# Performance work log

Measured on AMD Instinct MI355X. Metric: run time of the kernel, lower is better.

Reference implementation:

```python
import jax, jax.numpy as jnp
import numpy as np

B, T = 256, 800
D_IN, H, L, V = 128, 512, 2, 128


def setup_inputs() -> dict:
    key = jax.random.key(0)
    ks = jax.random.split(key, 12)
    s = 0.1  # init scale for stability
    return {
        "W_ih0": jax.random.normal(ks[0], (4 * H, D_IN), jnp.float32) * s,
        "W_hh0": jax.random.normal(ks[1], (4 * H, H), jnp.float32) * s,
        "b_ih0": jax.random.normal(ks[2], (4 * H,), jnp.float32) * s,
        "b_hh0": jax.random.normal(ks[3], (4 * H,), jnp.float32) * s,
        "W_ih1": jax.random.normal(ks[4], (4 * H, H), jnp.float32) * s,
        "W_hh1": jax.random.normal(ks[5], (4 * H, H), jnp.float32) * s,
        "b_ih1": jax.random.normal(ks[6], (4 * H,), jnp.float32) * s,
        "b_hh1": jax.random.normal(ks[7], (4 * H,), jnp.float32) * s,
        "W_lin": jax.random.normal(ks[8], (V, H), jnp.float32) * s,
        "b_lin": jax.random.normal(ks[9], (V,), jnp.float32) * s,
        "z": jax.random.randint(ks[10], (B, T), 0, V, jnp.int32),
        "num_frames": jax.random.randint(ks[11], (B,), 100, 800, jnp.int32),
    }


def _lstm_log_prob(layers, W_lin, b_lin, z, num_frames):
    # teacher-forced inputs: step i sees one_hot(z[:, i-1]), zeros at i=0
    oh = jax.nn.one_hot(z[:, :-1], D_IN, dtype=jnp.float32)          # [B, T-1, D]
    inputs = jnp.concatenate([jnp.zeros((B, 1, D_IN), jnp.float32), oh], axis=1)
    inputs = jnp.transpose(inputs, (1, 0, 2))                         # [T, B, D]

    def step(carry, x_t):
        h, c = carry  # each [L, B, H]
        inp = x_t
        hs, cs = [], []
        for l, (Wih, Whh, bih, bhh) in enumerate(layers):
            gates = inp @ Wih.T + h[l] @ Whh.T + bih + bhh            # [B, 4H]
            i, f, g, o = jnp.split(gates, 4, axis=-1)                 # torch gate order i,f,g,o
            c_new = jax.nn.sigmoid(f) * c[l] + jax.nn.sigmoid(i) * jnp.tanh(g)
            h_new = jax.nn.sigmoid(o) * jnp.tanh(c_new)
            hs.append(h_new)
            cs.append(c_new)
            inp = h_new
        logits_t = inp @ W_lin.T + b_lin                              # [B, V]
        return (jnp.stack(hs), jnp.stack(cs)), logits_t

    h0 = jnp.zeros((L, B, H), jnp.float32)
    c0 = jnp.zeros((L, B, H), jnp.float32)
    _, logits = jax.lax.scan(step, (h0, c0), inputs)                  # [T, B, V]
    logits = jnp.transpose(logits, (1, 0, 2))                         # [B, T, V]

    logp = jax.nn.log_softmax(logits, axis=-1)
    nll = -jnp.take_along_axis(logp, z[..., None].astype(jnp.int32), axis=-1)[..., 0]  # [B, T]
    mask = (jnp.arange(T)[None, :] < num_frames[:, None]).astype(nll.dtype)
    return (nll * mask).mean(axis=-1)                                 # [B] (mean over full T, as in torch)


def reference(W_ih0, W_hh0, b_ih0, b_hh0, W_ih1, W_hh1, b_ih1, b_hh1, W_lin, b_lin, z, num_frames):
    layers = [(W_ih0, W_hh0, b_ih0, b_hh0), (W_ih1, W_hh1, b_ih1, b_hh1)]
    return _lstm_log_prob(layers, W_lin, b_lin, z, num_frames)
```

## Files before the change

kernel.cpp:

```cpp
#include <hip/hip_runtime.h>

#define TT 800

typedef __attribute__((ext_vector_type(8))) short bf16x8;
typedef __attribute__((ext_vector_type(4))) float f32x4;
typedef unsigned short u16;
typedef unsigned int u32;
typedef unsigned long long u64;

constexpr int NCW = 128, NWG = 136, RT = 32;
constexpr size_t WL0A_OFF = 0;
constexpr size_t WL0B_OFF = 2097152;
constexpr size_t WL1_OFF  = 2621440;
constexpr size_t WLIN_OFF = 6815744;
constexpr size_t H0_OFF   = 6946816;
constexpr size_t H1_OFF   = 7471104;
constexpr size_t BAR_OFF  = 7995392;
constexpr int HB = 256 * 512;
constexpr int A_ST = 520;
constexpr int G_OFF_B = 33280;
constexpr int P_OFF_B = 49792;
constexpr int LDS_BYTES = 53248;

__device__ __forceinline__ u16 f2b(float x) {
  u32 u = __float_as_uint(x);
  return (u16)((u + 0x7FFFu + ((u >> 16) & 1u)) >> 16);
}
__device__ __forceinline__ float b2f(u16 v) { return __uint_as_float(((u32)v) << 16); }
__device__ __forceinline__ float sigf(float x) { return 1.f / (1.f + __expf(-x)); }
__device__ __forceinline__ float tanh_f(float x) { float e = __expf(2.f * x); return 1.f - 2.f / (e + 1.f); }

__device__ __forceinline__ u64 ld_coh8(const u64* p) {
  return __hip_atomic_load(p, __ATOMIC_RELAXED, __HIP_MEMORY_SCOPE_AGENT);
}
__device__ __forceinline__ void st_coh8(u64* p, u64 v) {
  __hip_atomic_store(p, v, __ATOMIC_RELAXED, __HIP_MEMORY_SCOPE_AGENT);
}
__device__ __forceinline__ void fadd(u32* f) {
  __hip_atomic_fetch_add(f, 1u, __ATOMIC_RELAXED, __HIP_MEMORY_SCOPE_AGENT);
}
__device__ __forceinline__ void fpoll(u32* f, u32 thr) {
  while (__hip_atomic_load(f, __ATOMIC_RELAXED, __HIP_MEMORY_SCOPE_AGENT) < thr)
    __builtin_amdgcn_s_sleep(1);
}

__global__ void prep_kernel(const float* __restrict__ wih0, const float* __restrict__ whh0,
                            const float* __restrict__ wih1, const float* __restrict__ whh1,
                            const float* __restrict__ wlinf,
                            u16* __restrict__ wl0a, u16* __restrict__ wl0b,
                            u16* __restrict__ wl1, u16* __restrict__ wlin) {
  int i = blockIdx.x * 256 + threadIdx.x;
  const int NA = 2048 * 512, NB = 128 * 2048, N1 = 2048 * 1024, N2 = 128 * 512;
  if (i < NA) {
    int col = i >> 9, k = i & 511;
    wl0a[i] = f2b(whh0[col * 512 + k]);
  } else if (i < NA + NB) {
    int j = i - NA, k = j >> 11, col = j & 2047;
    wl0b[j] = f2b(wih0[col * 128 + k]);
  } else if (i < NA + NB + N1) {
    int j = i - NA - NB, col = j >> 10, k = j & 1023;
    float v = (k < 512) ? wih1[col * 512 + k] : whh1[col * 512 + (k - 512)];
    wl1[j] = f2b(v);
  } else if (i < NA + NB + N1 + N2) {
    int j = i - NA - NB - N1, col = j >> 9, k = j & 511;
    wlin[j] = f2b(wlinf[col * 512 + k]);
  }
}

__global__ __launch_bounds__(256, 1) void lstm_kernel(
    const float* __restrict__ bih0, const float* __restrict__ bhh0,
    const float* __restrict__ bih1, const float* __restrict__ bhh1,
    const float* __restrict__ blin,
    const int* __restrict__ z, const int* __restrict__ nfr,
    const u16* __restrict__ wl0a, const u16* __restrict__ wl0b,
    const u16* __restrict__ wl1, const u16* __restrict__ wlin,
    u16* __restrict__ h0buf, u16* __restrict__ h1buf,
    u32* __restrict__ bars, float* __restrict__ out) {
  extern __shared__ char smem[];
  u16* A = (u16*)smem;
  float* Gf = (float*)(smem + G_OFF_B);
  float* Pm = (float*)(smem + P_OFF_B);
  float* Ps = Pm + 256;
  float* Pt = Ps + 256;
  const int wg = blockIdx.x;
  const int w_all = wg >> 3;
  const bool isC = (w_all < 16);
  const int tile = wg & 7;
  const int w = isC ? w_all : 16;
  const int tid = threadIdx.x, lane = tid & 63, wv = tid >> 6;
  const int l15 = lane & 15, l4 = lane >> 4;
  const int row0 = tile * RT;
  u32* F = bars + tile * 32;
  const f32x4 VZ = {0.f, 0.f, 0.f, 0.f};
  const int rC = tid >> 3, u0C = (tid & 7) * 4;
  const int cuL = tid & 31, rgL = tid >> 5;

  float c0s[4] = {0, 0, 0, 0}, c1s[4] = {0, 0, 0, 0};
  float accN = 0.f, nflv = 0.f;
  float bias0c[2], bias1c[2], biasLc[2];
  bf16x8 bq0R[32];
  bf16x8 bq1R[64];
  bf16x8 wlR[32];

  if (isC) {
#pragma unroll
    for (int cb = 0; cb < 2; ++cb) {
      int col = wv * 512 + w * 32 + cb * 16 + l15;
      bias0c[cb] = bih0[col] + bhh0[col];
      bias1c[cb] = bih1[col] + bhh1[col];
      const u16* b0 = wl0a + (size_t)col * 512 + l4 * 8;
#pragma unroll
      for (int kb = 0; kb < 16; ++kb) bq0R[cb * 16 + kb] = *(const bf16x8*)(b0 + kb * 32);
      const u16* b1 = wl1 + (size_t)col * 1024 + l4 * 8;
#pragma unroll
      for (int kb = 0; kb < 32; ++kb) bq1R[cb * 32 + kb] = *(const bf16x8*)(b1 + kb * 32);
    }
  } else {
#pragma unroll
    for (int cb = 0; cb < 2; ++cb) {
      int colV = wv * 32 + cb * 16 + l15;
      biasLc[cb] = blin[colV];
      const u16* bL = wlin + (size_t)colV * 512 + l4 * 8;
#pragma unroll
      for (int kb = 0; kb < 16; ++kb) wlR[cb * 16 + kb] = *(const bf16x8*)(bL + kb * 32);
    }
    if (rgL == 0) nflv = (float)nfr[row0 + cuL];
  }

  if (isC && w == 0) {
    u64* z0 = (u64*)(h0buf + HB + row0 * 512);
    u64* z1 = (u64*)(h1buf + row0 * 512);
    u64* z2 = (u64*)(h1buf + HB + row0 * 512);
    for (int k = tid; k < 2048; k += 256) { st_coh8(z0 + k, 0); st_coh8(z1 + k, 0); st_coh8(z2 + k, 0); }
  }
  __syncthreads();
  if (tid == 0) fadd(F);

  auto ldA = [&](int rb, int kb) {
    return *(const bf16x8*)(A + (rb * 16 + l15) * A_ST + kb * 32 + l4 * 8);
  };

#pragma unroll 1
  for (int tau = 0; tau <= TT + 1; ++tau) {
    if (tid == 0) fpoll(F, 17u * (u32)(tau + 1));
    __syncthreads();
    const u16* h0src = h0buf + ((tau + 1) & 1) * HB + row0 * 512;
    const u64* h1s64 = (const u64*)(h1buf + (tau & 1) * HB + row0 * 512);
    const bool l0act = isC && (tau < TT);
    const bool l1act = isC && (tau >= 1 && tau <= TT);

    if (isC) {
      if (tau <= TT) {
        u64 ta[8], tb[8];
        const u64* s64 = (const u64*)h0src;
#pragma unroll
        for (int c = 0; c < 8; ++c) {
          int li = c * 256 + tid;
          ta[c] = ld_coh8(s64 + li * 2); tb[c] = ld_coh8(s64 + li * 2 + 1);
        }
#pragma unroll
        for (int c = 0; c < 8; ++c) {
          int li = c * 256 + tid, row = li >> 6, cc = li & 63;
          u64* d = (u64*)(A + row * A_ST + cc * 8);
          d[0] = ta[c]; d[1] = tb[c];
        }
      }
      u64 ha[4], hb[4];
      if (l1act) {
#pragma unroll
        for (int c = 0; c < 4; ++c) {
          int li = c * 256 + tid;
          ha[c] = ld_coh8(h1s64 + li * 2); hb[c] = ld_coh8(h1s64 + li * 2 + 1);
        }
      }
      __syncthreads();

      f32x4 acc0[2][2] = {{VZ, VZ}, {VZ, VZ}};
      f32x4 acc1[2][2] = {{VZ, VZ}, {VZ, VZ}};
      if (l0act) {
#pragma unroll
        for (int kb = 0; kb < 16; ++kb) {
          bf16x8 a0 = ldA(0, kb), a1 = ldA(1, kb);
#pragma unroll
          for (int cb = 0; cb < 2; ++cb) {
            acc0[0][cb] = __builtin_amdgcn_mfma_f32_16x16x32_bf16(a0, bq0R[cb * 16 + kb], acc0[0][cb], 0, 0, 0);
            acc0[1][cb] = __builtin_amdgcn_mfma_f32_16x16x32_bf16(a1, bq0R[cb * 16 + kb], acc0[1][cb], 0, 0, 0);
          }
        }
      }
      if (l1act) {
#pragma unroll
        for (int kb = 0; kb < 16; ++kb) {
          bf16x8 a0 = ldA(0, kb), a1 = ldA(1, kb);
#pragma unroll
          for (int cb = 0; cb < 2; ++cb) {
            acc1[0][cb] = __builtin_amdgcn_mfma_f32_16x16x32_bf16(a0, bq1R[cb * 32 + kb], acc1[0][cb], 0, 0, 0);
            acc1[1][cb] = __builtin_amdgcn_mfma_f32_16x16x32_bf16(a1, bq1R[cb * 32 + kb], acc1[1][cb], 0, 0, 0);
          }
        }
      }
      if (l0act) {
#pragma unroll
        for (int rb = 0; rb < 2; ++rb)
#pragma unroll
          for (int cb = 0; cb < 2; ++cb)
#pragma unroll
            for (int q = 0; q < 4; ++q)
              Gf[(rb * 16 + l4 * 4 + q) * 129 + wv * 32 + cb * 16 + l15] = acc0[rb][cb][q] + bias0c[cb];
      }
      __syncthreads();

      u64 ha2[4], hb2[4];
      if (l1act) {
#pragma unroll
        for (int c = 0; c < 4; ++c) {
          int li = (c + 4) * 256 + tid;
          ha2[c] = ld_coh8(h1s64 + li * 2); hb2[c] = ld_coh8(h1s64 + li * 2 + 1);
        }
      }
      if (l0act) {
        float g4[4][4];
#pragma unroll
        for (int g = 0; g < 4; ++g)
#pragma unroll
          for (int j = 0; j < 4; ++j) g4[g][j] = Gf[rC * 129 + g * 32 + u0C + j];
        if (tau >= 1) {
          int zr = z[(row0 + rC) * TT + (tau - 1)];
          const u16* gb = wl0b + (size_t)zr * 2048 + w * 32 + u0C;
#pragma unroll
          for (int g = 0; g < 4; ++g) {
            u64 v = *(const u64*)(gb + g * 512);
#pragma unroll
            for (int j = 0; j < 4; ++j) g4[g][j] += b2f((u16)(v >> (16 * j)));
          }
        }
        u64 pk = 0;
#pragma unroll
        for (int j = 0; j < 4; ++j) {
          float cn = sigf(g4[1][j]) * c0s[j] + sigf(g4[0][j]) * tanh_f(g4[2][j]);
          float hn = sigf(g4[3][j]) * tanh_f(cn);
          c0s[j] = cn;
          pk |= ((u64)f2b(hn)) << (16 * j);
        }
        u16* h0w = h0buf + (tau & 1) * HB + row0 * 512;
        st_coh8((u64*)(h0w + rC * 512 + w * 32 + u0C), pk);
      }
      if (l1act) {
#pragma unroll
        for (int c = 0; c < 4; ++c) {
          int li = c * 256 + tid, row = li >> 6, cc = li & 63;
          u64* d = (u64*)(A + row * A_ST + cc * 8);
          d[0] = ha[c]; d[1] = hb[c];
        }
#pragma unroll
        for (int c = 0; c < 4; ++c) {
          int li = (c + 4) * 256 + tid, row = li >> 6, cc = li & 63;
          u64* d = (u64*)(A + row * A_ST + cc * 8);
          d[0] = ha2[c]; d[1] = hb2[c];
        }
      }
      __syncthreads();

      if (l1act) {
#pragma unroll
        for (int kb = 16; kb < 32; ++kb) {
          bf16x8 a0 = ldA(0, kb - 16), a1 = ldA(1, kb - 16);
#pragma unroll
          for (int cb = 0; cb < 2; ++cb) {
            acc1[0][cb] = __builtin_amdgcn_mfma_f32_16x16x32_bf16(a0, bq1R[cb * 32 + kb], acc1[0][cb], 0, 0, 0);
            acc1[1][cb] = __builtin_amdgcn_mfma_f32_16x16x32_bf16(a1, bq1R[cb * 32 + kb], acc1[1][cb], 0, 0, 0);
          }
        }
#pragma unroll
        for (int rb = 0; rb < 2; ++rb)
#pragma unroll
          for (int cb = 0; cb < 2; ++cb)
#pragma unroll
            for (int q = 0; q < 4; ++q)
              Gf[(rb * 16 + l4 * 4 + q) * 129 + wv * 32 + cb * 16 + l15] = acc1[rb][cb][q] + bias1c[cb];
      }
      __syncthreads();

      if (l1act) {
        float g4[4][4];
#pragma unroll
        for (int g = 0; g < 4; ++g)
#pragma unroll
          for (int j = 0; j < 4; ++j) g4[g][j] = Gf[rC * 129 + g * 32 + u0C + j];
        u64 pk = 0;
#pragma unroll
        for (int j = 0; j < 4; ++j) {
          float cn = sigf(g4[1][j]) * c1s[j] + sigf(g4[0][j]) * tanh_f(g4[2][j]);
          float hn = sigf(g4[3][j]) * tanh_f(cn);
          c1s[j] = cn;
          pk |= ((u64)f2b(hn)) << (16 * j);
        }
        u16* h1w = h1buf + ((tau + 1) & 1) * HB + row0 * 512;
        st_coh8((u64*)(h1w + rC * 512 + w * 32 + u0C), pk);
      }
      __syncthreads();
      if (tid == 0) fadd(F);
    } else {
      const bool lgact = (tau >= 2);
      if (lgact) {
        u64 ta[8], tb[8];
#pragma unroll
        for (int c = 0; c < 8; ++c) {
          int li = c * 256 + tid;
          ta[c] = ld_coh8(h1s64 + li * 2); tb[c] = ld_coh8(h1s64 + li * 2 + 1);
        }
#pragma unroll
        for (int c = 0; c < 8; ++c) {
          int li = c * 256 + tid, row = li >> 6, cc = li & 63;
          u64* d = (u64*)(A + row * A_ST + cc * 8);
          d[0] = ta[c]; d[1] = tb[c];
        }
      }
      __syncthreads();
      if (tid == 0) fadd(F);
      if (lgact) {
        f32x4 accL[2][2] = {{VZ, VZ}, {VZ, VZ}};
#pragma unroll
        for (int kb = 0; kb < 16; ++kb) {
          bf16x8 a0 = ldA(0, kb), a1 = ldA(1, kb);
#pragma unroll
          for (int cb = 0; cb < 2; ++cb) {
            accL[0][cb] = __builtin_amdgcn_mfma_f32_16x16x32_bf16(a0, wlR[cb * 16 + kb], accL[0][cb], 0, 0, 0);
            accL[1][cb] = __builtin_amdgcn_mfma_f32_16x16x32_bf16(a1, wlR[cb * 16 + kb], accL[1][cb], 0, 0, 0);
          }
        }
#pragma unroll
        for (int rb = 0; rb < 2; ++rb)
#pragma unroll
          for (int cb = 0; cb < 2; ++cb)
#pragma unroll
            for (int q = 0; q < 4; ++q)
              Gf[(rb * 16 + l4 * 4 + q) * 129 + wv * 32 + cb * 16 + l15] = accL[rb][cb][q] + biasLc[cb];
      }
      __syncthreads();
      if (lgact) {
        int t2 = tau - 2;
        int r = cuL, k = rgL;
        float vloc[16], mloc = -3.4e38f;
#pragma unroll
        for (int j = 0; j < 16; ++j) {
          vloc[j] = Gf[r * 129 + k * 16 + j];
          mloc = fmaxf(mloc, vloc[j]);
        }
        Pm[r * 8 + k] = mloc;
        __syncthreads();
        float mrow = Pm[r * 8];
#pragma unroll
        for (int j = 1; j < 8; ++j) mrow = fmaxf(mrow, Pm[r * 8 + j]);
        int zr = z[(row0 + r) * TT + t2];
        float sloc = 0.f, tloc = 0.f;
#pragma unroll
        for (int j = 0; j < 16; ++j) {
          sloc += __expf(vloc[j] - mrow);
          tloc += (k * 16 + j == zr) ? vloc[j] : 0.f;
        }
        Ps[r * 8 + k] = sloc; Pt[r * 8 + k] = tloc;
        __syncthreads();
        if (k == 0) {
          float s = 0.f, tv = 0.f;
#pragma unroll
          for (int j = 0; j < 8; ++j) { s += Ps[r * 8 + j]; tv += Pt[r * 8 + j]; }
          if ((float)t2 < nflv) accN += mrow + __logf(s) - tv;
        }
      } else {
        __syncthreads(); __syncthreads();
      }
    }
  }

  if (!isC && rgL == 0) out[row0 + cuL] = accN * (1.0f / TT);
}

extern "C" void kernel_launch(void* const* d_in, const int* in_sizes, int n_in,
                              void* d_out, int out_size, void* d_ws, size_t ws_size,
                              hipStream_t stream) {
  const float* wih0 = (const float*)d_in[0];
  const float* whh0 = (const float*)d_in[1];
  const float* bih0 = (const float*)d_in[2];
  const float* bhh0 = (const float*)d_in[3];
  const float* wih1 = (const float*)d_in[4];
  const float* whh1 = (const float*)d_in[5];
  const float* bih1 = (const float*)d_in[6];
  const float* bhh1 = (const float*)d_in[7];
  const float* wlinf = (const float*)d_in[8];
  const float* blin = (const float*)d_in[9];
  const int* z = (const int*)d_in[10];
  const int* nfr = (const int*)d_in[11];
  float* out = (float*)d_out;
  char* ws = (char*)d_ws;
  u16* wl0a = (u16*)(ws + WL0A_OFF);
  u16* wl0b = (u16*)(ws + WL0B_OFF);
  u16* wl1 = (u16*)(ws + WL1_OFF);
  u16* wlin = (u16*)(ws + WLIN_OFF);
  u16* h0buf = (u16*)(ws + H0_OFF);
  u16* h1buf = (u16*)(ws + H1_OFF);
  u32* bars = (u32*)(ws + BAR_OFF);

  hipMemsetAsync(ws + BAR_OFF, 0, 2048, stream);
  const int NTOT = 2048 * 512 + 128 * 2048 + 2048 * 1024 + 128 * 512;
  prep_kernel<<<dim3((NTOT + 255) / 256), dim3(256), 0, stream>>>(
      wih0, whh0, wih1, whh1, wlinf, wl0a, wl0b, wl1, wlin);
  lstm_kernel<<<dim3(NWG), dim3(256), LDS_BYTES, stream>>>(
      bih0, bhh0, bih1, bhh1, blin, z, nfr, wl0a, wl0b, wl1, wlin, h0buf, h1buf, bars, out);
}
```

Before: 8.631 ms.

## Use XCC-local coherence for per-tile flags and hidden-state exchange when co-located

```diff
diff --git a/kernel.cpp b/kernel.cpp
--- a/kernel.cpp
+++ b/kernel.cpp
@@ -43,6 +43,16 @@
   while (__hip_atomic_load(f, __ATOMIC_RELAXED, __HIP_MEMORY_SCOPE_AGENT) < thr)
     __builtin_amdgcn_s_sleep(1);
 }
+__device__ __forceinline__ void fadd_l(u32* f) {
+  __hip_atomic_fetch_add(f, 1u, __ATOMIC_RELAXED, __HIP_MEMORY_SCOPE_WORKGROUP);
+}
+__device__ __forceinline__ void fpoll_l(u32* f, u32 thr) {
+  while (*(volatile u32*)f < thr) {
+    __builtin_amdgcn_s_sleep(1);
+    asm volatile("buffer_inv" ::: "memory");
+  }
+}
+__device__ __forceinline__ void l1inv() { asm volatile("buffer_inv" ::: "memory"); }
 
 __global__ void prep_kernel(const float* __restrict__ wih0, const float* __restrict__ whh0,
                             const float* __restrict__ wih1, const float* __restrict__ whh1,
@@ -127,14 +137,37 @@
     if (rgL == 0) nflv = (float)nfr[row0 + cuL];
   }
 
+  u32 xcc;
+  asm volatile("s_getreg_b32 %0, hwreg(HW_REG_XCC_ID)" : "=s"(xcc));
+  {
+    int* hls = (int*)Pm;
+    if (tid == 0) {
+      u32 bit = 1u << (xcc & 31u);
+      __hip_atomic_fetch_or(bars + 256 + tile, bit, __ATOMIC_RELAXED, __HIP_MEMORY_SCOPE_AGENT);
+      __hip_atomic_fetch_add(bars + 272, 1u, __ATOMIC_RELAXED, __HIP_MEMORY_SCOPE_AGENT);
+      while (__hip_atomic_load(bars + 272, __ATOMIC_RELAXED, __HIP_MEMORY_SCOPE_AGENT) < (u32)NWG)
+        __builtin_amdgcn_s_sleep(1);
+      u32 m = __hip_atomic_load(bars + 256 + tile, __ATOMIC_RELAXED, __HIP_MEMORY_SCOPE_AGENT);
+      hls[0] = (m == bit) ? 1 : 0;
+    }
+    __syncthreads();
+    const_cast<volatile int&>(hls[0]);
+  }
+  const bool lok = (((volatile int*)Pm)[0] != 0);
+  __syncthreads();
+
   if (isC && w == 0) {
     u64* z0 = (u64*)(h0buf + HB + row0 * 512);
     u64* z1 = (u64*)(h1buf + row0 * 512);
     u64* z2 = (u64*)(h1buf + HB + row0 * 512);
-    for (int k = tid; k < 2048; k += 256) { st_coh8(z0 + k, 0); st_coh8(z1 + k, 0); st_coh8(z2 + k, 0); }
+    if (lok) {
+      for (int k = tid; k < 2048; k += 256) { z0[k] = 0; z1[k] = 0; z2[k] = 0; }
+    } else {
+      for (int k = tid; k < 2048; k += 256) { st_coh8(z0 + k, 0); st_coh8(z1 + k, 0); st_coh8(z2 + k, 0); }
+    }
   }
   __syncthreads();
-  if (tid == 0) fadd(F);
+  if (tid == 0) { if (lok) fadd_l(F); else fadd(F); }
 
   auto ldA = [&](int rb, int kb) {
     return *(const bf16x8*)(A + (rb * 16 + l15) * A_ST + kb * 32 + l4 * 8);
@@ -142,8 +175,9 @@
 
 #pragma unroll 1
   for (int tau = 0; tau <= TT + 1; ++tau) {
-    if (tid == 0) fpoll(F, 17u * (u32)(tau + 1));
+    if (tid == 0) { if (lok) fpoll_l(F, 17u * (u32)(tau + 1)); else fpoll(F, 17u * (u32)(tau + 1)); }
     __syncthreads();
+    if (lok) l1inv();
     const u16* h0src = h0buf + ((tau + 1) & 1) * HB + row0 * 512;
     const u64* h1s64 = (const u64*)(h1buf + (tau & 1) * HB + row0 * 512);
     const bool l0act = isC && (tau < TT);
@@ -153,10 +187,18 @@
       if (tau <= TT) {
         u64 ta[8], tb[8];
         const u64* s64 = (const u64*)h0src;
-#pragma unroll
-        for (int c = 0; c < 8; ++c) {
-          int li = c * 256 + tid;
-          ta[c] = ld_coh8(s64 + li * 2); tb[c] = ld_coh8(s64 + li * 2 + 1);
+        if (lok) {
+#pragma unroll
+          for (int c = 0; c < 8; ++c) {
+            int li = c * 256 + tid;
+            ta[c] = s64[li * 2]; tb[c] = s64[li * 2 + 1];
+          }
+        } else {
+#pragma unroll
+          for (int c = 0; c < 8; ++c) {
+            int li = c * 256 + tid;
+            ta[c] = ld_coh8(s64 + li * 2); tb[c] = ld_coh8(s64 + li * 2 + 1);
+          }
         }
 #pragma unroll
         for (int c = 0; c < 8; ++c) {
@@ -167,10 +209,18 @@
       }
       u64 ha[4], hb[4];
       if (l1act) {
-#pragma unroll
-        for (int c = 0; c < 4; ++c) {
-          int li = c * 256 + tid;
-          ha[c] = ld_coh8(h1s64 + li * 2); hb[c] = ld_coh8(h1s64 + li * 2 + 1);
+        if (lok) {
+#pragma unroll
+          for (int c = 0; c < 4; ++c) {
+            int li = c * 256 + tid;
+            ha[c] = h1s64[li * 2]; hb[c] = h1s64[li * 2 + 1];
+          }
+        } else {
+#pragma unroll
+          for (int c = 0; c < 4; ++c) {
+            int li = c * 256 + tid;
+            ha[c] = ld_coh8(h1s64 + li * 2); hb[c] = ld_coh8(h1s64 + li * 2 + 1);
+          }
         }
       }
       __syncthreads();
@@ -212,10 +262,18 @@
 
       u64 ha2[4], hb2[4];
       if (l1act) {
-#pragma unroll
-        for (int c = 0; c < 4; ++c) {
-          int li = (c + 4) * 256 + tid;
-          ha2[c] = ld_coh8(h1s64 + li * 2); hb2[c] = ld_coh8(h1s64 + li * 2 + 1);
+        if (lok) {
+#pragma unroll
+          for (int c = 0; c < 4; ++c) {
+            int li = (c + 4) * 256 + tid;
+            ha2[c] = h1s64[li * 2]; hb2[c] = h1s64[li * 2 + 1];
+          }
+        } else {
+#pragma unroll
+          for (int c = 0; c < 4; ++c) {
+            int li = (c + 4) * 256 + tid;
+            ha2[c] = ld_coh8(h1s64 + li * 2); hb2[c] = ld_coh8(h1s64 + li * 2 + 1);
+          }
         }
       }
       if (l0act) {
@@ -243,7 +301,8 @@
           pk |= ((u64)f2b(hn)) << (16 * j);
         }
         u16* h0w = h0buf + (tau & 1) * HB + row0 * 512;
-        st_coh8((u64*)(h0w + rC * 512 + w * 32 + u0C), pk);
+        u64* dst = (u64*)(h0w + rC * 512 + w * 32 + u0C);
+        if (lok) *dst = pk; else st_coh8(dst, pk);
       }
       if (l1act) {
 #pragma unroll
@@ -296,18 +355,27 @@
           pk |= ((u64)f2b(hn)) << (16 * j);
         }
         u16* h1w = h1buf + ((tau + 1) & 1) * HB + row0 * 512;
-        st_coh8((u64*)(h1w + rC * 512 + w * 32 + u0C), pk);
-      }
-      __syncthreads();
-      if (tid == 0) fadd(F);
+        u64* dst = (u64*)(h1w + rC * 512 + w * 32 + u0C);
+        if (lok) *dst = pk; else st_coh8(dst, pk);
+      }
+      __syncthreads();
+      if (tid == 0) { if (lok) fadd_l(F); else fadd(F); }
     } else {
       const bool lgact = (tau >= 2);
       if (lgact) {
         u64 ta[8], tb[8];
-#pragma unroll
-        for (int c = 0; c < 8; ++c) {
-          int li = c * 256 + tid;
-          ta[c] = ld_coh8(h1s64 + li * 2); tb[c] = ld_coh8(h1s64 + li * 2 + 1);
+        if (lok) {
+#pragma unroll
+          for (int c = 0; c < 8; ++c) {
+            int li = c * 256 + tid;
+            ta[c] = h1s64[li * 2]; tb[c] = h1s64[li * 2 + 1];
+          }
+        } else {
+#pragma unroll
+          for (int c = 0; c < 8; ++c) {
+            int li = c * 256 + tid;
+            ta[c] = ld_coh8(h1s64 + li * 2); tb[c] = ld_coh8(h1s64 + li * 2 + 1);
+          }
         }
 #pragma unroll
         for (int c = 0; c < 8; ++c) {
@@ -317,7 +385,7 @@
         }
       }
       __syncthreads();
-      if (tid == 0) fadd(F);
+      if (tid == 0) { if (lok) fadd_l(F); else fadd(F); }
       if (lgact) {
         f32x4 accL[2][2] = {{VZ, VZ}, {VZ, VZ}};
 #pragma unroll
```

Measured after the change: 7.665 ms. 11.2% less time.
